# Performance work log

Measured on AMD Instinct MI355X. Metric: run time of the kernel, lower is better.

Reference implementation:

```python
import jax, jax.numpy as jnp
import numpy as np

N_A, N_C, N_L = 50000, 10000, 10000
HID = 128


def _gatv2(x_src, x_dst, src, dst, ea, Wl, bl, Wr, br, We, att, bias, H):
    # GATv2Conv (PyG) bipartite, edge_dim=1, concat=False (mean over heads), eval mode (no dropout)
    C = bias.shape[0]
    n_dst = x_dst.shape[0]
    xl = (x_src @ Wl + bl).reshape(-1, H, C)      # [N_src, H, C]
    xr = (x_dst @ Wr + br).reshape(-1, H, C)      # [N_dst, H, C]
    e = jax.nn.leaky_relu(xl[src] + xr[dst] + (ea @ We).reshape(-1, H, C), 0.2)  # [E,H,C]
    logit = jnp.einsum('ehc,hc->eh', e, att)      # [E,H]
    m = jax.ops.segment_max(logit, dst, num_segments=n_dst)
    m = jax.lax.stop_gradient(jnp.where(jnp.isfinite(m), m, 0.0))
    ex = jnp.exp(logit - m[dst])
    denom = jax.ops.segment_sum(ex, dst, num_segments=n_dst)
    alpha = ex / (denom[dst] + 1e-16)             # segment softmax over incoming edges
    out = jax.ops.segment_sum(alpha[:, :, None] * xl[src], dst, num_segments=n_dst)
    return out.mean(axis=1) + bias                # concat=False -> head mean + bias


def setup_inputs() -> dict:
    key = jax.random.key(0)
    ks = iter(jax.random.split(key, 80))
    def rn(shape, s=1.0):
        return jax.random.normal(next(ks), shape, jnp.float32) * s
    inp = {}
    inp['x_asset'] = rn((N_A, 512))
    inp['x_creator'] = rn((N_C, 2))
    inp['x_licensee'] = rn((N_L, 1))
    # edges: (name, E, src_max, dst_max)
    edges = [('cb', 50000, N_A, N_C), ('lt', 100000, N_A, N_L), ('sim', 200000, N_A, N_A),
             ('fw', 100000, N_A, N_A), ('rcb', 50000, N_C, N_A), ('rlt', 100000, N_L, N_A)]
    for name, E, smax, dmax in edges:
        inp[f'{name}_src'] = jax.random.randint(next(ks), (E,), 0, smax, jnp.int32)
        inp[f'{name}_dst'] = jax.random.randint(next(ks), (E,), 0, dmax, jnp.int32)
        inp[f'ea_{name}'] = rn((E, 1))
    w = 0.05  # param scale
    inp['Wp_a'] = rn((512, HID), w); inp['bp_a'] = rn((HID,), w)
    inp['Wp_c'] = rn((2, HID), w);   inp['bp_c'] = rn((HID,), w)
    inp['Wp_l'] = rn((1, HID), w);   inp['bp_l'] = rn((HID,), w)
    # layer 1: heads=2, stacked over the 6 relations
    H1 = 2
    inp['Wl1'] = rn((6, HID, H1 * HID), w); inp['bl1'] = rn((6, H1 * HID), w)
    inp['Wr1'] = rn((6, HID, H1 * HID), w); inp['br1'] = rn((6, H1 * HID), w)
    inp['We1'] = rn((6, 1, H1 * HID), w)
    inp['att1'] = rn((6, H1, HID), w); inp['bias1'] = rn((6, HID), w)
    # layer 2: heads=1
    inp['Wl2'] = rn((6, HID, HID), w); inp['bl2'] = rn((6, HID), w)
    inp['Wr2'] = rn((6, HID, HID), w); inp['br2'] = rn((6, HID), w)
    inp['We2'] = rn((6, 1, HID), w)
    inp['att2'] = rn((6, 1, HID), w); inp['bias2'] = rn((6, HID), w)
    inp['Wc1'] = rn((HID, HID), w); inp['bc1'] = rn((HID,), w)
    inp['Wc2'] = rn((HID, 3), w);   inp['bc2'] = rn((3,), w)
    inp['query_asset_index'] = 123
    return inp


def reference(x_asset, x_creator, x_licensee, Wp_a, bp_a, Wp_c, bp_c, Wp_l, bp_l,
              Wl1, bl1, Wr1, br1, We1, att1, bias1,
              Wl2, bl2, Wr2, br2, We2, att2, bias2,
              Wc1, bc1, Wc2, bc2,
              ea_cb, ea_lt, ea_sim, ea_fw, ea_rcb, ea_rlt,
              cb_src, cb_dst, lt_src, lt_dst, sim_src, sim_dst,
              fw_src, fw_dst, rcb_src, rcb_dst, rlt_src, rlt_dst,
              query_asset_index):
    x = {'Asset': x_asset @ Wp_a + bp_a,
         'Creator': x_creator @ Wp_c + bp_c,
         'Licensee': x_licensee @ Wp_l + bp_l}
    rels = [('Asset', 'Creator', cb_src, cb_dst, ea_cb),
            ('Asset', 'Licensee', lt_src, lt_dst, ea_lt),
            ('Asset', 'Asset', sim_src, sim_dst, ea_sim),
            ('Asset', 'Asset', fw_src, fw_dst, ea_fw),
            ('Creator', 'Asset', rcb_src, rcb_dst, ea_rcb),
            ('Licensee', 'Asset', rlt_src, rlt_dst, ea_rlt)]

    def hetero_layer(x, Wl, bl, Wr, br, We, att, bias, H):
        out = {k: jnp.zeros((v.shape[0], HID), v.dtype) for k, v in x.items()}
        for i, (st, dt, s, d, ea) in enumerate(rels):  # HeteroConv aggr='sum'
            out[dt] = out[dt] + _gatv2(x[st], x[dt], s, d, ea,
                                       Wl[i], bl[i], Wr[i], br[i], We[i], att[i], bias[i], H)
        return out

    x = hetero_layer(x, Wl1, bl1, Wr1, br1, We1, att1, bias1, 2)
    x = {k: jax.nn.relu(v) for k, v in x.items()}  # eval: dropout is identity
    x = hetero_layer(x, Wl2, bl2, Wr2, br2, We2, att2, bias2, 1)
    x = {k: jax.nn.relu(v) for k, v in x.items()}
    a = x['Asset'][query_asset_index]
    return jax.nn.relu(a @ Wc1 + bc1) @ Wc2 + bc2
```

## Files before the change

kernel.cpp:

```cpp
#include <hip/hip_runtime.h>
#include <math.h>

#define FAMAX 64
#define FCMAX 32
#define FLMAX 32
#define N1MAX 512
#define N2MAX 128

struct Inputs {
  const float *x_asset, *x_creator, *x_licensee;
  const float *Wp_a,*bp_a,*Wp_c,*bp_c,*Wp_l,*bp_l;
  const float *Wl1,*bl1,*Wr1,*br1,*We1,*att1,*bias1;
  const float *Wl2,*bl2,*Wr2,*br2,*We2,*att2,*bias2;
  const float *Wc1,*bc1,*Wc2,*bc2;
};

struct Edges {
  const int *cb_s,*cb_d;  const float* ea_cb;  int Ecb;
  const int *lt_s,*lt_d;  const float* ea_lt;  int Elt;
  const int *sim_s,*sim_d;const float* ea_sim; int Esim;
  const int *fw_s,*fw_d;  const float* ea_fw;  int Efw;
  const int *rcb_s,*rcb_d;const float* ea_rcb; int Ercb;
  const int *rlt_s,*rlt_d;const float* ea_rlt; int Erlt;
};

struct WSP {
  int* cnt;
  int *dfA,*dfC,*dfL;
  int *fa,*fc,*fl;
  int* l2rel; int* l2src; float* l2ea;
  int* l1rel; int* l1src; int* l1dslot; float* l1ea;
  float* xl1e;
  float* logit1;
  float *x1a,*x1c,*x1l;
  float* xl2e;
  float* logit2;
};

__device__ __forceinline__ float leaky(float x){ return x > 0.f ? x : 0.2f*x; }

__device__ __forceinline__ void claim(int* flag, int* cnt, int* list, int node, int cap){
  int old = atomicCAS(&flag[node], 0, 1);
  if (old == 0){
    int k = atomicAdd(cnt, 1);
    if (k < cap){ list[k] = node; atomicExch(&flag[node], k + 2); }
    else atomicExch(&flag[node], 0);
  }
}

__device__ __forceinline__ void proj256(int type, int node, const Inputs& in,
                                        float* h0, float* xs, float* part){
  int t = threadIdx.x;
  if (type == 0){
    xs[t]       = in.x_asset[(size_t)node*512 + t];
    xs[t + 256] = in.x_asset[(size_t)node*512 + t + 256];
    __syncthreads();
    int j = t & 127, g2 = t >> 7;
    float acc = 0.f;
    const float* W = in.Wp_a + (size_t)g2*256*128 + j;
    const float* xg = xs + g2*256;
    for (int k=0;k<256;k++) acc = fmaf(xg[k], W[(size_t)k*128], acc);
    part[t] = acc;
    __syncthreads();
    if (t < 128) h0[t] = in.bp_a[t] + part[t] + part[128 + t];
  } else if (type == 1){
    if (t < 128)
      h0[t] = in.bp_c[t] + in.x_creator[node*2]*in.Wp_c[t]
            + in.x_creator[node*2+1]*in.Wp_c[128+t];
  } else {
    if (t < 128)
      h0[t] = in.bp_l[t] + in.x_licensee[node]*in.Wp_l[t];
  }
  __syncthreads();
}

__global__ void k1_scan_l2(Edges eg, const int* qptr, WSP w){
  int q = qptr[0];
  if (blockIdx.x==0 && threadIdx.x==0) claim(w.dfA, &w.cnt[1], w.fa, q, FAMAX);
  int total = eg.Esim + eg.Efw + eg.Ercb + eg.Erlt;
  for (int i = blockIdx.x*blockDim.x + threadIdx.x; i < total; i += gridDim.x*blockDim.x){
    int j = i, rel; const int *sp,*dp; const float* ep;
    if (j < eg.Esim){ rel=2; sp=eg.sim_s; dp=eg.sim_d; ep=eg.ea_sim; }
    else { j -= eg.Esim;
      if (j < eg.Efw){ rel=3; sp=eg.fw_s; dp=eg.fw_d; ep=eg.ea_fw; }
      else { j -= eg.Efw;
        if (j < eg.Ercb){ rel=4; sp=eg.rcb_s; dp=eg.rcb_d; ep=eg.ea_rcb; }
        else { j -= eg.Ercb; rel=5; sp=eg.rlt_s; dp=eg.rlt_d; ep=eg.ea_rlt; }
      }
    }
    if (dp[j] == q){
      int src = sp[j];
      int k = atomicAdd(&w.cnt[0], 1);
      if (k < N2MAX){ w.l2rel[k]=rel; w.l2src[k]=src; w.l2ea[k]=ep[j]; }
      if (rel <= 3) claim(w.dfA,&w.cnt[1],w.fa,src,FAMAX);
      else if (rel == 4) claim(w.dfC,&w.cnt[2],w.fc,src,FCMAX);
      else claim(w.dfL,&w.cnt[3],w.fl,src,FLMAX);
    }
  }
}

__global__ void k2_scan_l1(Edges eg, WSP w){
  int total = eg.Ecb+eg.Elt+eg.Esim+eg.Efw+eg.Ercb+eg.Erlt;
  for (int i = blockIdx.x*blockDim.x + threadIdx.x; i < total; i += gridDim.x*blockDim.x){
    int j = i, rel; const int *sp,*dp; const float* ep; const int* flag;
    if (j < eg.Ecb){ rel=0; sp=eg.cb_s; dp=eg.cb_d; ep=eg.ea_cb; flag=w.dfC; }
    else { j -= eg.Ecb;
    if (j < eg.Elt){ rel=1; sp=eg.lt_s; dp=eg.lt_d; ep=eg.ea_lt; flag=w.dfL; }
    else { j -= eg.Elt;
    if (j < eg.Esim){ rel=2; sp=eg.sim_s; dp=eg.sim_d; ep=eg.ea_sim; flag=w.dfA; }
    else { j -= eg.Esim;
    if (j < eg.Efw){ rel=3; sp=eg.fw_s; dp=eg.fw_d; ep=eg.ea_fw; flag=w.dfA; }
    else { j -= eg.Efw;
    if (j < eg.Ercb){ rel=4; sp=eg.rcb_s; dp=eg.rcb_d; ep=eg.ea_rcb; flag=w.dfA; }
    else { j -= eg.Ercb; rel=5; sp=eg.rlt_s; dp=eg.rlt_d; ep=eg.ea_rlt; flag=w.dfA; }}}}}
    int f = flag[dp[j]];
    if (f >= 2){
      int k = atomicAdd(&w.cnt[4], 1);
      if (k < N1MAX){ w.l1rel[k]=rel; w.l1src[k]=sp[j]; w.l1dslot[k]=f-2; w.l1ea[k]=ep[j]; }
    }
  }
}

__global__ void k3_edge(Inputs in, WSP w){
  __shared__ float xs[512];
  __shared__ float part[256];
  __shared__ float h0s[128];
  __shared__ float h0d[128];
  __shared__ float red[256];
  int i = blockIdx.x, t = threadIdx.x;
  int n1 = w.cnt[4] < N1MAX ? w.cnt[4] : N1MAX;
  if (i >= n1) return;
  int rel = w.l1rel[i], src = w.l1src[i], dslot = w.l1dslot[i];
  float ea = w.l1ea[i];
  int stype = (rel <= 3) ? 0 : (rel == 4 ? 1 : 2);
  int dtype = (rel == 0) ? 1 : (rel == 1 ? 2 : 0);
  int dnode = (rel == 0) ? w.fc[dslot] : (rel == 1 ? w.fl[dslot] : w.fa[dslot]);
  proj256(stype, src, in, h0s, xs, part);
  float xl1 = in.bl1[rel*256 + t];
  {
    const float* W = in.Wl1 + (size_t)rel*128*256 + t;
    for (int c=0;c<128;c++) xl1 = fmaf(h0s[c], W[(size_t)c*256], xl1);
  }
  w.xl1e[(size_t)i*256 + t] = xl1;
  proj256(dtype, dnode, in, h0d, xs, part);
  float xr1 = in.br1[rel*256 + t];
  {
    const float* W = in.Wr1 + (size_t)rel*128*256 + t;
    for (int c=0;c<128;c++) xr1 = fmaf(h0d[c], W[(size_t)c*256], xr1);
  }
  int h = t >> 7, c = t & 127;
  float e = leaky(xl1 + xr1 + ea*in.We1[rel*256 + t]);
  red[t] = e * in.att1[(rel*2 + h)*128 + c];
  __syncthreads();
  for (int s=64; s>0; s>>=1){ if (c < s) red[t] += red[t+s]; __syncthreads(); }
  if (c == 0) w.logit1[i*2 + h] = red[t];
}

__global__ void k4_agg(Inputs in, WSP w){
  int b = blockIdx.x, j = threadIdx.x;
  int nfa = w.cnt[1] < FAMAX ? w.cnt[1] : FAMAX;
  int nfc = w.cnt[2] < FCMAX ? w.cnt[2] : FCMAX;
  int nfl = w.cnt[3] < FLMAX ? w.cnt[3] : FLMAX;
  int type, slot;
  if (b < FAMAX){ slot=b; if (slot>=nfa) return; type=0; }
  else if (b < FAMAX+FCMAX){ slot=b-FAMAX; if (slot>=nfc) return; type=1; }
  else { slot=b-FAMAX-FCMAX; if (slot>=nfl) return; type=2; }
  int n1 = w.cnt[4] < N1MAX ? w.cnt[4] : N1MAX;
  float out = 0.f;
  int r0, r1;
  if (type==0){ r0=2; r1=5; } else if (type==1){ r0=0; r1=0; } else { r0=1; r1=1; }
  for (int r=r0; r<=r1; r++){
    out += in.bias1[r*128 + j];
    float m0=-INFINITY, m1=-INFINITY;
    for (int i=0;i<n1;i++){
      if (w.l1rel[i]==r && w.l1dslot[i]==slot){
        m0 = fmaxf(m0, w.logit1[i*2]);
        m1 = fmaxf(m1, w.logit1[i*2+1]);
      }
    }
    if (m0 == -INFINITY) continue;
    float d0=0.f, d1=0.f, a0=0.f, a1=0.f;
    for (int i=0;i<n1;i++){
      if (w.l1rel[i]==r && w.l1dslot[i]==slot){
        float e0 = expf(w.logit1[i*2]   - m0);
        float e1 = expf(w.logit1[i*2+1] - m1);
        d0 += e0; d1 += e1;
        a0 = fmaf(e0, w.xl1e[(size_t)i*256 + j],       a0);
        a1 = fmaf(e1, w.xl1e[(size_t)i*256 + 128 + j], a1);
      }
    }
    out += 0.5f*(a0/(d0+1e-16f) + a1/(d1+1e-16f));
  }
  float v = fmaxf(out, 0.f);
  if (type==0) w.x1a[slot*128 + j] = v;
  else if (type==1) w.x1c[slot*128 + j] = v;
  else w.x1l[slot*128 + j] = v;
}

__global__ void k5b_l2edge(Inputs in, WSP w, const int* qptr){
  __shared__ float xq[128];
  __shared__ float xsrc[128];
  __shared__ float red[128];
  int i = blockIdx.x, j = threadIdx.x;
  int n2 = w.cnt[0] < N2MAX ? w.cnt[0] : N2MAX;
  if (i >= n2) return;
  int rel = w.l2rel[i], src = w.l2src[i];
  float ea = w.l2ea[i];
  int f; const float* xb;
  if (rel <= 3){ f = w.dfA[src]; xb = w.x1a; }
  else if (rel == 4){ f = w.dfC[src]; xb = w.x1c; }
  else { f = w.dfL[src]; xb = w.x1l; }
  if (f < 2){
    w.xl2e[(size_t)i*128 + j] = 0.f;
    if (j == 0) w.logit2[i] = -INFINITY;
    return;
  }
  int q = qptr[0];
  int qs = w.dfA[q] - 2;
  xq[j]   = w.x1a[(size_t)qs*128 + j];
  xsrc[j] = xb[(size_t)(f-2)*128 + j];
  __syncthreads();
  float xr2 = in.br2[rel*128 + j];
  {
    const float* W = in.Wr2 + (size_t)rel*128*128 + j;
    for (int c=0;c<128;c++) xr2 = fmaf(xq[c], W[(size_t)c*128], xr2);
  }
  float xl2 = in.bl2[rel*128 + j];
  {
    const float* W = in.Wl2 + (size_t)rel*128*128 + j;
    for (int c=0;c<128;c++) xl2 = fmaf(xsrc[c], W[(size_t)c*128], xl2);
  }
  w.xl2e[(size_t)i*128 + j] = xl2;
  float e = leaky(xl2 + xr2 + ea*in.We2[rel*128 + j]);
  red[j] = e * in.att2[rel*128 + j];
  __syncthreads();
  for (int s=64; s>0; s>>=1){ if (j < s) red[j] += red[j+s]; __syncthreads(); }
  if (j == 0) w.logit2[i] = red[0];
}

__global__ void k5c_final(Inputs in, WSP w, float* outp){
  __shared__ float x2[128];
  __shared__ float tt[128];
  int j = threadIdx.x;
  int n2 = w.cnt[0] < N2MAX ? w.cnt[0] : N2MAX;
  float o = 0.f;
  for (int r=2; r<=5; r++){
    o += in.bias2[r*128 + j];
    float m = -INFINITY;
    for (int i=0;i<n2;i++) if (w.l2rel[i]==r) m = fmaxf(m, w.logit2[i]);
    if (m == -INFINITY) continue;
    float d = 0.f, acc = 0.f;
    for (int i=0;i<n2;i++) if (w.l2rel[i]==r){
      float e = expf(w.logit2[i] - m);
      d += e;
      acc = fmaf(e, w.xl2e[(size_t)i*128 + j], acc);
    }
    o += acc/(d + 1e-16f);
  }
  x2[j] = fmaxf(o, 0.f);
  __syncthreads();
  float acc = in.bc1[j];
  for (int c=0;c<128;c++) acc = fmaf(x2[c], in.Wc1[c*128 + j], acc);
  tt[j] = fmaxf(acc, 0.f);
  __syncthreads();
  if (j < 3){
    float r = in.bc2[j];
    for (int c=0;c<128;c++) r = fmaf(tt[c], in.Wc2[c*3 + j], r);
    outp[j] = r;
  }
}

extern "C" void kernel_launch(void* const* d_in, const int* in_sizes, int n_in,
                              void* d_out, int out_size, void* d_ws, size_t ws_size,
                              hipStream_t stream){
  Inputs in;
  in.x_asset   = (const float*)d_in[0];
  in.x_creator = (const float*)d_in[1];
  in.x_licensee= (const float*)d_in[2];
  Edges eg;
  eg.cb_s =(const int*)d_in[3];  eg.cb_d =(const int*)d_in[4];  eg.ea_cb =(const float*)d_in[5];  eg.Ecb = in_sizes[3];
  eg.lt_s =(const int*)d_in[6];  eg.lt_d =(const int*)d_in[7];  eg.ea_lt =(const float*)d_in[8];  eg.Elt = in_sizes[6];
  eg.sim_s=(const int*)d_in[9];  eg.sim_d=(const int*)d_in[10]; eg.ea_sim=(const float*)d_in[11]; eg.Esim= in_sizes[9];
  eg.fw_s =(const int*)d_in[12]; eg.fw_d =(const int*)d_in[13]; eg.ea_fw =(const float*)d_in[14]; eg.Efw = in_sizes[12];
  eg.rcb_s=(const int*)d_in[15]; eg.rcb_d=(const int*)d_in[16]; eg.ea_rcb=(const float*)d_in[17]; eg.Ercb= in_sizes[15];
  eg.rlt_s=(const int*)d_in[18]; eg.rlt_d=(const int*)d_in[19]; eg.ea_rlt=(const float*)d_in[20]; eg.Erlt= in_sizes[18];
  in.Wp_a=(const float*)d_in[21]; in.bp_a=(const float*)d_in[22];
  in.Wp_c=(const float*)d_in[23]; in.bp_c=(const float*)d_in[24];
  in.Wp_l=(const float*)d_in[25]; in.bp_l=(const float*)d_in[26];
  in.Wl1=(const float*)d_in[27]; in.bl1=(const float*)d_in[28];
  in.Wr1=(const float*)d_in[29]; in.br1=(const float*)d_in[30];
  in.We1=(const float*)d_in[31]; in.att1=(const float*)d_in[32]; in.bias1=(const float*)d_in[33];
  in.Wl2=(const float*)d_in[34]; in.bl2=(const float*)d_in[35];
  in.Wr2=(const float*)d_in[36]; in.br2=(const float*)d_in[37];
  in.We2=(const float*)d_in[38]; in.att2=(const float*)d_in[39]; in.bias2=(const float*)d_in[40];
  in.Wc1=(const float*)d_in[41]; in.bc1=(const float*)d_in[42];
  in.Wc2=(const float*)d_in[43]; in.bc2=(const float*)d_in[44];
  const int* qptr = (const int*)d_in[45];

  char* p = (char*)d_ws;
  auto carve = [&](size_t n)->char*{ char* r = p; p += ((n + 255) & ~(size_t)255); return r; };
  WSP w;
  w.cnt  = (int*)carve(16*4);
  w.dfA  = (int*)carve(50000*4); w.dfC = (int*)carve(10000*4); w.dfL = (int*)carve(10000*4);
  size_t zero_bytes = (size_t)(p - (char*)d_ws);
  w.fa = (int*)carve(FAMAX*4); w.fc = (int*)carve(FCMAX*4); w.fl = (int*)carve(FLMAX*4);
  w.l2rel=(int*)carve(N2MAX*4); w.l2src=(int*)carve(N2MAX*4); w.l2ea=(float*)carve(N2MAX*4);
  w.l1rel=(int*)carve(N1MAX*4); w.l1src=(int*)carve(N1MAX*4); w.l1dslot=(int*)carve(N1MAX*4); w.l1ea=(float*)carve(N1MAX*4);
  w.xl1e=(float*)carve((size_t)N1MAX*256*4);
  w.logit1=(float*)carve((size_t)N1MAX*2*4);
  w.x1a=(float*)carve((size_t)FAMAX*128*4);
  w.x1c=(float*)carve((size_t)FCMAX*128*4);
  w.x1l=(float*)carve((size_t)FLMAX*128*4);
  w.xl2e=(float*)carve((size_t)N2MAX*128*4);
  w.logit2=(float*)carve(N2MAX*4);

  hipMemsetAsync(d_ws, 0, zero_bytes, stream);

  int tE2 = eg.Esim + eg.Efw + eg.Ercb + eg.Erlt;
  k1_scan_l2<<<(tE2+255)/256, 256, 0, stream>>>(eg, qptr, w);
  int tE1 = eg.Ecb + eg.Elt + tE2;
  k2_scan_l1<<<(tE1+255)/256, 256, 0, stream>>>(eg, w);
  k3_edge<<<N1MAX, 256, 0, stream>>>(in, w);
  k4_agg<<<FAMAX + FCMAX + FLMAX, 128, 0, stream>>>(in, w);
  k5b_l2edge<<<N2MAX, 128, 0, stream>>>(in, w, qptr);
  k5c_final<<<1, 128, 0, stream>>>(in, w, (float*)d_out);
}
```

Baseline: 305.4 us.

## Fuse all stages into one cooperative persistent kernel with grid syncs

Replaces six kernel launches and the workspace memset with a single cooperative kernel of 256 blocks that moves between phases using grid.sync. The global atomic flag arrays for frontier dedup are replaced by a serial per-block list built in shared memory and a linear search over small frontier lists. The layer-2 edge work and the final head run in one block, with the query-side projection computed once per relation. This removes launch and memset overhead, but the scans now run on fewer threads with linear slot searches, and the layer-2 edges are processed serially in one block.

After: 615.0 us. 101% more time.

```diff
diff --git a/kernel.cpp b/kernel.cpp
--- a/kernel.cpp
+++ b/kernel.cpp
@@ -1,11 +1,16 @@
 #include <hip/hip_runtime.h>
+#include <hip/hip_cooperative_groups.h>
 #include <math.h>
+
+namespace cg = cooperative_groups;
 
 #define FAMAX 64
 #define FCMAX 32
 #define FLMAX 32
 #define N1MAX 512
 #define N2MAX 128
+#define NBLK  256
+#define NTHR  256
 
 struct Inputs {
   const float *x_asset, *x_creator, *x_licensee;
@@ -26,27 +31,15 @@
 
 struct WSP {
   int* cnt;
-  int *dfA,*dfC,*dfL;
-  int *fa,*fc,*fl;
   int* l2rel; int* l2src; float* l2ea;
   int* l1rel; int* l1src; int* l1dslot; float* l1ea;
   float* xl1e;
   float* logit1;
   float *x1a,*x1c,*x1l;
   float* xl2e;
-  float* logit2;
 };
 
 __device__ __forceinline__ float leaky(float x){ return x > 0.f ? x : 0.2f*x; }
-
-__device__ __forceinline__ void claim(int* flag, int* cnt, int* list, int node, int cap){
-  int old = atomicCAS(&flag[node], 0, 1);
-  if (old == 0){
-    int k = atomicAdd(cnt, 1);
-    if (k < cap){ list[k] = node; atomicExch(&flag[node], k + 2); }
-    else atomicExch(&flag[node], 0);
-  }
-}
 
 __device__ __forceinline__ void proj256(int type, int node, const Inputs& in,
                                         float* h0, float* xs, float* part){
@@ -74,199 +67,265 @@
   __syncthreads();
 }
 
-__global__ void k1_scan_l2(Edges eg, const int* qptr, WSP w){
-  int q = qptr[0];
-  if (blockIdx.x==0 && threadIdx.x==0) claim(w.dfA, &w.cnt[1], w.fa, q, FAMAX);
-  int total = eg.Esim + eg.Efw + eg.Ercb + eg.Erlt;
-  for (int i = blockIdx.x*blockDim.x + threadIdx.x; i < total; i += gridDim.x*blockDim.x){
-    int j = i, rel; const int *sp,*dp; const float* ep;
-    if (j < eg.Esim){ rel=2; sp=eg.sim_s; dp=eg.sim_d; ep=eg.ea_sim; }
-    else { j -= eg.Esim;
-      if (j < eg.Efw){ rel=3; sp=eg.fw_s; dp=eg.fw_d; ep=eg.ea_fw; }
-      else { j -= eg.Efw;
-        if (j < eg.Ercb){ rel=4; sp=eg.rcb_s; dp=eg.rcb_d; ep=eg.ea_rcb; }
-        else { j -= eg.Ercb; rel=5; sp=eg.rlt_s; dp=eg.rlt_d; ep=eg.ea_rlt; }
-      }
-    }
-    if (dp[j] == q){
-      int src = sp[j];
-      int k = atomicAdd(&w.cnt[0], 1);
-      if (k < N2MAX){ w.l2rel[k]=rel; w.l2src[k]=src; w.l2ea[k]=ep[j]; }
-      if (rel <= 3) claim(w.dfA,&w.cnt[1],w.fa,src,FAMAX);
-      else if (rel == 4) claim(w.dfC,&w.cnt[2],w.fc,src,FCMAX);
-      else claim(w.dfL,&w.cnt[3],w.fl,src,FLMAX);
-    }
-  }
-}
-
-__global__ void k2_scan_l1(Edges eg, WSP w){
-  int total = eg.Ecb+eg.Elt+eg.Esim+eg.Efw+eg.Ercb+eg.Erlt;
-  for (int i = blockIdx.x*blockDim.x + threadIdx.x; i < total; i += gridDim.x*blockDim.x){
-    int j = i, rel; const int *sp,*dp; const float* ep; const int* flag;
-    if (j < eg.Ecb){ rel=0; sp=eg.cb_s; dp=eg.cb_d; ep=eg.ea_cb; flag=w.dfC; }
-    else { j -= eg.Ecb;
-    if (j < eg.Elt){ rel=1; sp=eg.lt_s; dp=eg.lt_d; ep=eg.ea_lt; flag=w.dfL; }
-    else { j -= eg.Elt;
-    if (j < eg.Esim){ rel=2; sp=eg.sim_s; dp=eg.sim_d; ep=eg.ea_sim; flag=w.dfA; }
-    else { j -= eg.Esim;
-    if (j < eg.Efw){ rel=3; sp=eg.fw_s; dp=eg.fw_d; ep=eg.ea_fw; flag=w.dfA; }
-    else { j -= eg.Efw;
-    if (j < eg.Ercb){ rel=4; sp=eg.rcb_s; dp=eg.rcb_d; ep=eg.ea_rcb; flag=w.dfA; }
-    else { j -= eg.Ercb; rel=5; sp=eg.rlt_s; dp=eg.rlt_d; ep=eg.ea_rlt; flag=w.dfA; }}}}}
-    int f = flag[dp[j]];
-    if (f >= 2){
-      int k = atomicAdd(&w.cnt[4], 1);
-      if (k < N1MAX){ w.l1rel[k]=rel; w.l1src[k]=sp[j]; w.l1dslot[k]=f-2; w.l1ea[k]=ep[j]; }
-    }
-  }
-}
-
-__global__ void k3_edge(Inputs in, WSP w){
+__global__ void __launch_bounds__(NTHR)
+mega(Inputs in, Edges eg, WSP w, const int* qptr, float* outp){
   __shared__ float xs[512];
   __shared__ float part[256];
   __shared__ float h0s[128];
   __shared__ float h0d[128];
   __shared__ float red[256];
-  int i = blockIdx.x, t = threadIdx.x;
-  int n1 = w.cnt[4] < N1MAX ? w.cnt[4] : N1MAX;
-  if (i >= n1) return;
-  int rel = w.l1rel[i], src = w.l1src[i], dslot = w.l1dslot[i];
-  float ea = w.l1ea[i];
-  int stype = (rel <= 3) ? 0 : (rel == 4 ? 1 : 2);
-  int dtype = (rel == 0) ? 1 : (rel == 1 ? 2 : 0);
-  int dnode = (rel == 0) ? w.fc[dslot] : (rel == 1 ? w.fl[dslot] : w.fa[dslot]);
-  proj256(stype, src, in, h0s, xs, part);
-  float xl1 = in.bl1[rel*256 + t];
-  {
-    const float* W = in.Wl1 + (size_t)rel*128*256 + t;
-    for (int c=0;c<128;c++) xl1 = fmaf(h0s[c], W[(size_t)c*256], xl1);
-  }
-  w.xl1e[(size_t)i*256 + t] = xl1;
-  proj256(dtype, dnode, in, h0d, xs, part);
-  float xr1 = in.br1[rel*256 + t];
-  {
-    const float* W = in.Wr1 + (size_t)rel*128*256 + t;
-    for (int c=0;c<128;c++) xr1 = fmaf(h0d[c], W[(size_t)c*256], xr1);
-  }
-  int h = t >> 7, c = t & 127;
-  float e = leaky(xl1 + xr1 + ea*in.We1[rel*256 + t]);
-  red[t] = e * in.att1[(rel*2 + h)*128 + c];
-  __syncthreads();
-  for (int s=64; s>0; s>>=1){ if (c < s) red[t] += red[t+s]; __syncthreads(); }
-  if (c == 0) w.logit1[i*2 + h] = red[t];
-}
-
-__global__ void k4_agg(Inputs in, WSP w){
-  int b = blockIdx.x, j = threadIdx.x;
-  int nfa = w.cnt[1] < FAMAX ? w.cnt[1] : FAMAX;
-  int nfc = w.cnt[2] < FCMAX ? w.cnt[2] : FCMAX;
-  int nfl = w.cnt[3] < FLMAX ? w.cnt[3] : FLMAX;
-  int type, slot;
-  if (b < FAMAX){ slot=b; if (slot>=nfa) return; type=0; }
-  else if (b < FAMAX+FCMAX){ slot=b-FAMAX; if (slot>=nfc) return; type=1; }
-  else { slot=b-FAMAX-FCMAX; if (slot>=nfl) return; type=2; }
-  int n1 = w.cnt[4] < N1MAX ? w.cnt[4] : N1MAX;
-  float out = 0.f;
-  int r0, r1;
-  if (type==0){ r0=2; r1=5; } else if (type==1){ r0=0; r1=0; } else { r0=1; r1=1; }
-  for (int r=r0; r<=r1; r++){
-    out += in.bias1[r*128 + j];
-    float m0=-INFINITY, m1=-INFINITY;
-    for (int i=0;i<n1;i++){
-      if (w.l1rel[i]==r && w.l1dslot[i]==slot){
-        m0 = fmaxf(m0, w.logit1[i*2]);
-        m1 = fmaxf(m1, w.logit1[i*2+1]);
-      }
-    }
-    if (m0 == -INFINITY) continue;
-    float d0=0.f, d1=0.f, a0=0.f, a1=0.f;
-    for (int i=0;i<n1;i++){
-      if (w.l1rel[i]==r && w.l1dslot[i]==slot){
-        float e0 = expf(w.logit1[i*2]   - m0);
-        float e1 = expf(w.logit1[i*2+1] - m1);
-        d0 += e0; d1 += e1;
-        a0 = fmaf(e0, w.xl1e[(size_t)i*256 + j],       a0);
-        a1 = fmaf(e1, w.xl1e[(size_t)i*256 + 128 + j], a1);
-      }
-    }
-    out += 0.5f*(a0/(d0+1e-16f) + a1/(d1+1e-16f));
-  }
-  float v = fmaxf(out, 0.f);
-  if (type==0) w.x1a[slot*128 + j] = v;
-  else if (type==1) w.x1c[slot*128 + j] = v;
-  else w.x1l[slot*128 + j] = v;
-}
-
-__global__ void k5b_l2edge(Inputs in, WSP w, const int* qptr){
-  __shared__ float xq[128];
-  __shared__ float xsrc[128];
-  __shared__ float red[128];
-  int i = blockIdx.x, j = threadIdx.x;
-  int n2 = w.cnt[0] < N2MAX ? w.cnt[0] : N2MAX;
-  if (i >= n2) return;
-  int rel = w.l2rel[i], src = w.l2src[i];
-  float ea = w.l2ea[i];
-  int f; const float* xb;
-  if (rel <= 3){ f = w.dfA[src]; xb = w.x1a; }
-  else if (rel == 4){ f = w.dfC[src]; xb = w.x1c; }
-  else { f = w.dfL[src]; xb = w.x1l; }
-  if (f < 2){
-    w.xl2e[(size_t)i*128 + j] = 0.f;
-    if (j == 0) w.logit2[i] = -INFINITY;
-    return;
-  }
-  int q = qptr[0];
-  int qs = w.dfA[q] - 2;
-  xq[j]   = w.x1a[(size_t)qs*128 + j];
-  xsrc[j] = xb[(size_t)(f-2)*128 + j];
-  __syncthreads();
-  float xr2 = in.br2[rel*128 + j];
-  {
-    const float* W = in.Wr2 + (size_t)rel*128*128 + j;
-    for (int c=0;c<128;c++) xr2 = fmaf(xq[c], W[(size_t)c*128], xr2);
-  }
-  float xl2 = in.bl2[rel*128 + j];
-  {
-    const float* W = in.Wl2 + (size_t)rel*128*128 + j;
-    for (int c=0;c<128;c++) xl2 = fmaf(xsrc[c], W[(size_t)c*128], xl2);
-  }
-  w.xl2e[(size_t)i*128 + j] = xl2;
-  float e = leaky(xl2 + xr2 + ea*in.We2[rel*128 + j]);
-  red[j] = e * in.att2[rel*128 + j];
-  __syncthreads();
-  for (int s=64; s>0; s>>=1){ if (j < s) red[j] += red[j+s]; __syncthreads(); }
-  if (j == 0) w.logit2[i] = red[0];
-}
-
-__global__ void k5c_final(Inputs in, WSP w, float* outp){
-  __shared__ float x2[128];
-  __shared__ float tt[128];
-  int j = threadIdx.x;
-  int n2 = w.cnt[0] < N2MAX ? w.cnt[0] : N2MAX;
-  float o = 0.f;
-  for (int r=2; r<=5; r++){
-    o += in.bias2[r*128 + j];
-    float m = -INFINITY;
-    for (int i=0;i<n2;i++) if (w.l2rel[i]==r) m = fmaxf(m, w.logit2[i]);
-    if (m == -INFINITY) continue;
-    float d = 0.f, acc = 0.f;
-    for (int i=0;i<n2;i++) if (w.l2rel[i]==r){
-      float e = expf(w.logit2[i] - m);
-      d += e;
-      acc = fmaf(e, w.xl2e[(size_t)i*128 + j], acc);
-    }
-    o += acc/(d + 1e-16f);
-  }
-  x2[j] = fmaxf(o, 0.f);
-  __syncthreads();
-  float acc = in.bc1[j];
-  for (int c=0;c<128;c++) acc = fmaf(x2[c], in.Wc1[c*128 + j], acc);
-  tt[j] = fmaxf(acc, 0.f);
-  __syncthreads();
-  if (j < 3){
-    float r = in.bc2[j];
-    for (int c=0;c<128;c++) r = fmaf(tt[c], in.Wc2[c*3 + j], r);
-    outp[j] = r;
+  __shared__ float s_xr2[4*128];
+  __shared__ int   s_fa[FAMAX];
+  __shared__ int   s_fc[FCMAX];
+  __shared__ int   s_fl[FLMAX];
+  __shared__ int   s_nf[3];
+  __shared__ int   s_l2slot[N2MAX];
+  __shared__ int   s_l2src[N2MAX];
+  __shared__ int   s_key[N1MAX];
+  __shared__ float s_lg0[N1MAX];
+  __shared__ float s_lg1[N1MAX];
+
+  cg::grid_group grid = cg::this_grid();
+  const int t = threadIdx.x;
+  const int b = blockIdx.x;
+  const int gtid = b*NTHR + t;
+  const int gstride = NBLK*NTHR;
+  const int q = qptr[0];
+
+  if (b == 0 && t < 16) w.cnt[t] = 0;
+  grid.sync();
+
+  {
+    int total = eg.Esim + eg.Efw + eg.Ercb + eg.Erlt;
+    for (int i = gtid; i < total; i += gstride){
+      int j = i, rel; const int *sp,*dp; const float* ep;
+      if (j < eg.Esim){ rel=2; sp=eg.sim_s; dp=eg.sim_d; ep=eg.ea_sim; }
+      else { j -= eg.Esim;
+        if (j < eg.Efw){ rel=3; sp=eg.fw_s; dp=eg.fw_d; ep=eg.ea_fw; }
+        else { j -= eg.Efw;
+          if (j < eg.Ercb){ rel=4; sp=eg.rcb_s; dp=eg.rcb_d; ep=eg.ea_rcb; }
+          else { j -= eg.Ercb; rel=5; sp=eg.rlt_s; dp=eg.rlt_d; ep=eg.ea_rlt; }
+        }
+      }
+      if (dp[j] == q){
+        int k = atomicAdd(&w.cnt[0], 1);
+        if (k < N2MAX){ w.l2rel[k]=rel; w.l2src[k]=sp[j]; w.l2ea[k]=ep[j]; }
+      }
+    }
+  }
+  grid.sync();
+
+  {
+    int n2 = min(w.cnt[0], N2MAX);
+    for (int i = t; i < n2; i += NTHR){
+      s_key[i]   = w.l2rel[i];
+      s_l2src[i] = w.l2src[i];
+    }
+    __syncthreads();
+    if (t == 0){
+      int nfa = 0, nfc = 0, nfl = 0;
+      s_fa[nfa++] = q;
+      for (int i=0;i<n2;i++){
+        int rel = s_key[i], src = s_l2src[i];
+        int s = -1;
+        if (rel <= 3){
+          for (int k=0;k<nfa;k++) if (s_fa[k]==src){ s=k; break; }
+          if (s < 0 && nfa < FAMAX){ s = nfa; s_fa[nfa++] = src; }
+        } else if (rel == 4){
+          for (int k=0;k<nfc;k++) if (s_fc[k]==src){ s=k; break; }
+          if (s < 0 && nfc < FCMAX){ s = nfc; s_fc[nfc++] = src; }
+        } else {
+          for (int k=0;k<nfl;k++) if (s_fl[k]==src){ s=k; break; }
+          if (s < 0 && nfl < FLMAX){ s = nfl; s_fl[nfl++] = src; }
+        }
+        s_l2slot[i] = s;
+      }
+      s_nf[0]=nfa; s_nf[1]=nfc; s_nf[2]=nfl;
+    }
+    __syncthreads();
+  }
+
+  {
+    int nfa = s_nf[0], nfc = s_nf[1], nfl = s_nf[2];
+    int total = eg.Ecb+eg.Elt+eg.Esim+eg.Efw+eg.Ercb+eg.Erlt;
+    for (int i = gtid; i < total; i += gstride){
+      int j = i, rel; const int *sp,*dp; const float* ep;
+      if (j < eg.Ecb){ rel=0; sp=eg.cb_s; dp=eg.cb_d; ep=eg.ea_cb; }
+      else { j -= eg.Ecb;
+      if (j < eg.Elt){ rel=1; sp=eg.lt_s; dp=eg.lt_d; ep=eg.ea_lt; }
+      else { j -= eg.Elt;
+      if (j < eg.Esim){ rel=2; sp=eg.sim_s; dp=eg.sim_d; ep=eg.ea_sim; }
+      else { j -= eg.Esim;
+      if (j < eg.Efw){ rel=3; sp=eg.fw_s; dp=eg.fw_d; ep=eg.ea_fw; }
+      else { j -= eg.Efw;
+      if (j < eg.Ercb){ rel=4; sp=eg.rcb_s; dp=eg.rcb_d; ep=eg.ea_rcb; }
+      else { j -= eg.Ercb; rel=5; sp=eg.rlt_s; dp=eg.rlt_d; ep=eg.ea_rlt; }}}}}
+      int d = dp[j];
+      int slot = -1;
+      if (rel == 0){ for (int k=0;k<nfc;k++) if (s_fc[k]==d){ slot=k; break; } }
+      else if (rel == 1){ for (int k=0;k<nfl;k++) if (s_fl[k]==d){ slot=k; break; } }
+      else { for (int k=0;k<nfa;k++) if (s_fa[k]==d){ slot=k; break; } }
+      if (slot >= 0){
+        int k = atomicAdd(&w.cnt[4], 1);
+        if (k < N1MAX){ w.l1rel[k]=rel; w.l1src[k]=sp[j]; w.l1dslot[k]=slot; w.l1ea[k]=ep[j]; }
+      }
+    }
+  }
+  grid.sync();
+
+  {
+    int n1 = min(w.cnt[4], N1MAX);
+    for (int e = b; e < n1; e += NBLK){
+      int rel = w.l1rel[e], src = w.l1src[e], dslot = w.l1dslot[e];
+      float ea = w.l1ea[e];
+      int stype = (rel <= 3) ? 0 : (rel == 4 ? 1 : 2);
+      int dtype = (rel == 0) ? 1 : (rel == 1 ? 2 : 0);
+      int dnode = (rel == 0) ? s_fc[dslot] : (rel == 1 ? s_fl[dslot] : s_fa[dslot]);
+      proj256(stype, src, in, h0s, xs, part);
+      float xl1 = in.bl1[rel*256 + t];
+      {
+        const float* W = in.Wl1 + (size_t)rel*128*256 + t;
+        for (int c=0;c<128;c++) xl1 = fmaf(h0s[c], W[(size_t)c*256], xl1);
+      }
+      w.xl1e[(size_t)e*256 + t] = xl1;
+      proj256(dtype, dnode, in, h0d, xs, part);
+      float xr1 = in.br1[rel*256 + t];
+      {
+        const float* W = in.Wr1 + (size_t)rel*128*256 + t;
+        for (int c=0;c<128;c++) xr1 = fmaf(h0d[c], W[(size_t)c*256], xr1);
+      }
+      int h = t >> 7, c = t & 127;
+      float ev = leaky(xl1 + xr1 + ea*in.We1[rel*256 + t]);
+      red[t] = ev * in.att1[(rel*2 + h)*128 + c];
+      __syncthreads();
+      for (int s=64; s>0; s>>=1){ if (c < s) red[t] += red[t+s]; __syncthreads(); }
+      if (c == 0) w.logit1[e*2 + h] = red[t];
+      __syncthreads();
+    }
+  }
+  grid.sync();
+
+  {
+    int n1 = min(w.cnt[4], N1MAX);
+    int nfa = s_nf[0], nfc = s_nf[1], nfl = s_nf[2];
+    int nf = nfa + nfc + nfl;
+    if (b < nf){
+      for (int i = t; i < n1; i += NTHR){
+        s_key[i] = (w.l1rel[i] << 8) | w.l1dslot[i];
+        s_lg0[i] = w.logit1[i*2];
+        s_lg1[i] = w.logit1[i*2+1];
+      }
+      __syncthreads();
+      if (t < 128){
+        int type, slot;
+        if (b < nfa){ type=0; slot=b; }
+        else if (b < nfa+nfc){ type=1; slot=b-nfa; }
+        else { type=2; slot=b-nfa-nfc; }
+        int r0, r1;
+        if (type==0){ r0=2; r1=5; } else if (type==1){ r0=0; r1=0; } else { r0=1; r1=1; }
+        float out = 0.f;
+        for (int r=r0; r<=r1; r++){
+          out += in.bias1[r*128 + t];
+          int key = (r<<8) | slot;
+          float m0=-INFINITY, m1=-INFINITY;
+          for (int i=0;i<n1;i++){
+            if (s_key[i]==key){
+              m0 = fmaxf(m0, s_lg0[i]);
+              m1 = fmaxf(m1, s_lg1[i]);
+            }
+          }
+          if (m0 == -INFINITY) continue;
+          float d0=0.f, d1=0.f, a0=0.f, a1=0.f;
+          for (int i=0;i<n1;i++){
+            if (s_key[i]==key){
+              float e0 = expf(s_lg0[i] - m0);
+              float e1 = expf(s_lg1[i] - m1);
+              d0 += e0; d1 += e1;
+              a0 = fmaf(e0, w.xl1e[(size_t)i*256 + t],       a0);
+              a1 = fmaf(e1, w.xl1e[(size_t)i*256 + 128 + t], a1);
+            }
+          }
+          out += 0.5f*(a0/(d0+1e-16f) + a1/(d1+1e-16f));
+        }
+        float v = fmaxf(out, 0.f);
+        if (type==0) w.x1a[slot*128 + t] = v;
+        else if (type==1) w.x1c[slot*128 + t] = v;
+        else w.x1l[slot*128 + t] = v;
+      }
+    }
+  }
+  grid.sync();
+
+  if (b == 0){
+    int n2 = min(w.cnt[0], N2MAX);
+    for (int i = t; i < n2; i += NTHR){
+      s_key[i] = w.l2rel[i];
+      s_lg1[i] = w.l2ea[i];
+    }
+    if (t < 128) h0s[t] = w.x1a[t];
+    __syncthreads();
+    int j = t & 127, g = t >> 7;
+    for (int r=2; r<=5; r++){
+      const float* W = in.Wr2 + (size_t)r*128*128 + j;
+      float acc = 0.f;
+      for (int c=g*64; c<g*64+64; c++) acc = fmaf(h0s[c], W[(size_t)c*128], acc);
+      part[t] = acc;
+      __syncthreads();
+      if (t < 128) s_xr2[(r-2)*128 + t] = in.br2[r*128 + t] + part[t] + part[t+128];
+      __syncthreads();
+    }
+    for (int i=0; i<n2; i++){
+      int rel = s_key[i];
+      int slot = s_l2slot[i];
+      float ea = s_lg1[i];
+      const float* xb = (rel <= 3) ? w.x1a : (rel == 4 ? w.x1c : w.x1l);
+      if (t < 128) h0d[t] = (slot >= 0) ? xb[(size_t)slot*128 + t] : 0.f;
+      __syncthreads();
+      const float* W = in.Wl2 + (size_t)rel*128*128 + j;
+      float acc = 0.f;
+      for (int c=g*64; c<g*64+64; c++) acc = fmaf(h0d[c], W[(size_t)c*128], acc);
+      part[t] = acc;
+      __syncthreads();
+      if (t < 128){
+        float xl2 = in.bl2[rel*128 + t] + part[t] + part[t+128];
+        w.xl2e[(size_t)i*128 + t] = xl2;
+        float ev = leaky(xl2 + s_xr2[(rel-2)*128 + t] + ea*in.We2[rel*128 + t]);
+        red[t] = ev * in.att2[rel*128 + t];
+      }
+      __syncthreads();
+      for (int s=64; s>0; s>>=1){ if (t < s) red[t] += red[t+s]; __syncthreads(); }
+      if (t == 0) s_lg0[i] = (slot >= 0) ? red[0] : -INFINITY;
+      __syncthreads();
+    }
+    if (t < 128){
+      float o = 0.f;
+      for (int r=2; r<=5; r++){
+        o += in.bias2[r*128 + t];
+        float m = -INFINITY;
+        for (int i=0;i<n2;i++) if (s_key[i]==r) m = fmaxf(m, s_lg0[i]);
+        if (m == -INFINITY) continue;
+        float dsum = 0.f, acc = 0.f;
+        for (int i=0;i<n2;i++) if (s_key[i]==r){
+          float e = expf(s_lg0[i] - m);
+          dsum += e;
+          acc = fmaf(e, w.xl2e[(size_t)i*128 + t], acc);
+        }
+        o += acc/(dsum + 1e-16f);
+      }
+      h0d[t] = fmaxf(o, 0.f);
+    }
+    __syncthreads();
+    if (t < 128){
+      float acc = in.bc1[t];
+      for (int c=0;c<128;c++) acc = fmaf(h0d[c], in.Wc1[c*128 + t], acc);
+      red[t] = fmaxf(acc, 0.f);
+    }
+    __syncthreads();
+    if (t < 3){
+      float r = in.bc2[t];
+      for (int c=0;c<128;c++) r = fmaf(red[c], in.Wc2[c*3 + t], r);
+      outp[t] = r;
+    }
   }
 }
 
@@ -296,14 +355,12 @@
   in.Wc1=(const float*)d_in[41]; in.bc1=(const float*)d_in[42];
   in.Wc2=(const float*)d_in[43]; in.bc2=(const float*)d_in[44];
   const int* qptr = (const int*)d_in[45];
+  float* outp = (float*)d_out;
 
   char* p = (char*)d_ws;
   auto carve = [&](size_t n)->char*{ char* r = p; p += ((n + 255) & ~(size_t)255); return r; };
   WSP w;
   w.cnt  = (int*)carve(16*4);
-  w.dfA  = (int*)carve(50000*4); w.dfC = (int*)carve(10000*4); w.dfL = (int*)carve(10000*4);
-  size_t zero_bytes = (size_t)(p - (char*)d_ws);
-  w.fa = (int*)carve(FAMAX*4); w.fc = (int*)carve(FCMAX*4); w.fl = (int*)carve(FLMAX*4);
   w.l2rel=(int*)carve(N2MAX*4); w.l2src=(int*)carve(N2MAX*4); w.l2ea=(float*)carve(N2MAX*4);
   w.l1rel=(int*)carve(N1MAX*4); w.l1src=(int*)carve(N1MAX*4); w.l1dslot=(int*)carve(N1MAX*4); w.l1ea=(float*)carve(N1MAX*4);
   w.xl1e=(float*)carve((size_t)N1MAX*256*4);
@@ -312,16 +369,7 @@
   w.x1c=(float*)carve((size_t)FCMAX*128*4);
   w.x1l=(float*)carve((size_t)FLMAX*128*4);
   w.xl2e=(float*)carve((size_t)N2MAX*128*4);
-  w.logit2=(float*)carve(N2MAX*4);
-
-  hipMemsetAsync(d_ws, 0, zero_bytes, stream);
-
-  int tE2 = eg.Esim + eg.Efw + eg.Ercb + eg.Erlt;
-  k1_scan_l2<<<(tE2+255)/256, 256, 0, stream>>>(eg, qptr, w);
-  int tE1 = eg.Ecb + eg.Elt + tE2;
-  k2_scan_l1<<<(tE1+255)/256, 256, 0, stream>>>(eg, w);
-  k3_edge<<<N1MAX, 256, 0, stream>>>(in, w);
-  k4_agg<<<FAMAX + FCMAX + FLMAX, 128, 0, stream>>>(in, w);
-  k5b_l2edge<<<N2MAX, 128, 0, stream>>>(in, w, qptr);
-  k5c_final<<<1, 128, 0, stream>>>(in, w, (float*)d_out);
+
+  void* args[] = { (void*)&in, (void*)&eg, (void*)&w, (void*)&qptr, (void*)&outp };
+  hipLaunchCooperativeKernel(mega, dim3(NBLK), dim3(NTHR), args, 0, stream);
 }
```
